# Optimization experiments

Hardware: AMD Instinct MI355X
Metric: run time of the kernel (lower is better)

Reference implementation:

```python
import jax, jax.numpy as jnp
import numpy as np

B, N, F, D, C = 4096, 8, 64, 64, 10  # batch, carriages, phys dim, bond dim, output classes


def setup_inputs() -> dict:
    key = jax.random.key(0)
    k1, k2, k3, k4 = jax.random.split(key, 4)
    scale = 1.0 / np.sqrt(F * D)
    x = jax.random.normal(k1, (B, N, F), dtype=jnp.float32)
    core_first = jax.random.normal(k2, (C, F, D), dtype=jnp.float32) * scale  # A1: (left=1 squeezed, up=C, p=F, right=D)
    cores_mid = jax.random.normal(k3, (N - 2, D, F, D), dtype=jnp.float32) * scale  # A2..A7: (D, up=1 squeezed, F, D)
    core_last = jax.random.normal(k4, (D, F), dtype=jnp.float32) * scale  # A8: (D, up=1, F, right=1 squeezed)
    return {"x": x, "core_first": core_first, "cores_mid": cores_mid, "core_last": core_last}


def reference(x, core_first, cores_mid, core_last):
    # Tensor-train forward: out[s, c] = sum over bond chain of
    #   A1[c, p1, r1] x[s,0,p1] * prod_i A_i[l, p_i, r] x[s,i,p_i] * A_N[l, p_N] x[s,N-1,p_N]
    # First carriage: contract physical leg -> (B, C, D)
    T0 = jnp.einsum('sp,cpr->scr', x[:, 0], core_first)
    # Middle carriages: sequential chain of small bond-dim GEMMs via scan
    xs_mid = jnp.moveaxis(x[:, 1:-1], 1, 0)  # (N-2, B, F)

    def step(T, inp):
        xi, core = inp  # xi: (B, F), core: (D, F, D)
        M = jnp.einsum('sp,lpr->slr', xi, core)  # (B, D, D)
        return jnp.einsum('scl,slr->scr', T, M), None

    T, _ = jax.lax.scan(step, T0, (xs_mid, cores_mid))
    # Last carriage: contract physical and close the chain -> (B, C)
    m_last = jnp.einsum('sp,lp->sl', x[:, -1], core_last)  # (B, D)
    out = jnp.einsum('scl,sl->sc', T, m_last)
    return out
```

## Files before the change

### kernel.cpp

```cpp
#include <hip/hip_runtime.h>


typedef _Float16 half8 __attribute__((ext_vector_type(8)));
typedef _Float16 half4 __attribute__((ext_vector_type(4)));
typedef _Float16 half2v __attribute__((ext_vector_type(2)));
typedef float f32x4 __attribute__((ext_vector_type(4)));

#define LAST_OFF   0
#define MID_OFF    4096
#define MID_SZ     262144
#define FIRST_OFF  1576960
#define N_FRAGS    3208

__global__ __launch_bounds__(256) void tt_swz(
    const float* __restrict__ cf,
    const float* __restrict__ cm,
    const float* __restrict__ cl,
    _Float16* __restrict__ ws)
{
  int gid = blockIdx.x * 256 + threadIdx.x;
  if (gid >= N_FRAGS * 64) return;
  int lane = gid & 63, frag = gid >> 6;
  int quad = lane >> 4, m16 = lane & 15;
  half8 hv;
  _Float16* dst;
  if (frag < 8) {
    int t = frag >> 1, kt = frag & 1;
    int l = t * 16 + m16;
    const float* s = cl + l * 64 + kt * 32 + quad * 8;
#pragma unroll
    for (int j = 0; j < 8; ++j) hv[j] = (_Float16)s[j];
    dst = ws + LAST_OFF + (size_t)((t * 2 + kt) * 64 + lane) * 8;
  } else if (frag < 8 + 3072) {
    int f2 = frag - 8;
    int ci = f2 >> 9, rem = f2 & 511;
    int t = rem >> 1, kt = rem & 1;
    int l = (t & 3) * 16 + m16, p = t >> 2;
    const float* s = cm + (((size_t)ci * 64 + l) * 64 + p) * 64 + kt * 32 + quad * 8;
#pragma unroll
    for (int j = 0; j < 8; ++j) hv[j] = (_Float16)s[j];
    dst = ws + MID_OFF + (size_t)ci * MID_SZ + (size_t)(rem * 64 + lane) * 8;
  } else {
    int f2 = frag - 3080;
    int t = f2 >> 1, kt = f2 & 1;
    int c = m16, p = t;
    if (c < 10) {
      const float* s = cf + ((size_t)(c * 64 + p)) * 64 + kt * 32 + quad * 8;
#pragma unroll
      for (int j = 0; j < 8; ++j) hv[j] = (_Float16)s[j];
    } else {
#pragma unroll
      for (int j = 0; j < 8; ++j) hv[j] = (_Float16)0.f;
    }
    dst = ws + FIRST_OFF + (size_t)((t * 2 + kt) * 64 + lane) * 8;
  }
  *(half8*)dst = hv;
}

__global__ __launch_bounds__(1024) void tt_main(
    const float* __restrict__ x,
    const _Float16* __restrict__ ws,
    float* __restrict__ out)
{
  __shared__ __align__(16) _Float16 Xs[512][33];
  __shared__ __align__(16) _Float16 Vt[4][32][72];
  __shared__ __align__(16) _Float16 Vc[32][72];
  const int tid = threadIdx.x;
  const int w = tid >> 6, lane = tid & 63;
  const int quad = lane >> 4, sl = lane & 15;
  const int blk = blockIdx.x;

  {
    const float* xb = x + (size_t)blk * 32 * 512;
    int s = tid >> 5, q = tid & 31;
#pragma unroll
    for (int k = 0; k < 4; ++k) {
      int f4 = q + 32 * k;
      float4 v = *(const float4*)(xb + (size_t)s * 512 + (size_t)f4 * 4);
      int row = f4 * 4;
      Xs[row + 0][s] = (_Float16)v.x;
      Xs[row + 1][s] = (_Float16)v.y;
      Xs[row + 2][s] = (_Float16)v.z;
      Xs[row + 3][s] = (_Float16)v.w;
    }
    _Float16* vz = &Vt[2][0][0];
    for (int idx = tid; idx < 2 * 32 * 72; idx += 1024) vz[idx] = (_Float16)0.f;
  }
  __syncthreads();

  {
    int st = w >> 3, kt = (w >> 2) & 1, tt = w & 3;
    half8 b;
#pragma unroll
    for (int j = 0; j < 8; ++j)
      b[j] = Xs[448 + kt * 32 + quad * 8 + j][st * 16 + sl];
    half8 a = *(const half8*)(ws + LAST_OFF + (size_t)((tt * 2 + kt) * 64 + lane) * 8);
    f32x4 d = {0.f, 0.f, 0.f, 0.f};
    d = __builtin_amdgcn_mfma_f32_16x16x32_f16(a, b, d, 0, 0, 0);
    half4 hv;
#pragma unroll
    for (int r = 0; r < 4; ++r) hv[r] = (_Float16)d[r];
    *(half4*)&Vt[kt][st * 16 + sl][tt * 16 + quad * 4] = hv;
  }
  __syncthreads();
  {
    int s = tid >> 5, rp = tid & 31;
    float r0 = 0.f, r1 = 0.f;
#pragma unroll
    for (int p = 0; p < 4; ++p) {
      half2v h = *(const half2v*)&Vt[p][s][rp * 2];
      r0 += (float)h[0]; r1 += (float)h[1];
    }
    half2v o; o[0] = (_Float16)r0; o[1] = (_Float16)r1;
    *(half2v*)&Vc[s][rp * 2] = o;
  }
  __syncthreads();

  const int g = w & 3, part = w >> 2;
  for (int step = 0; step < 6; ++step) {
    int ci = 5 - step;
    half8 b00 = *(const half8*)&Vc[sl][quad * 8];
    half8 b01 = *(const half8*)&Vc[sl][32 + quad * 8];
    half8 b10 = *(const half8*)&Vc[16 + sl][quad * 8];
    half8 b11 = *(const half8*)&Vc[16 + sl][32 + quad * 8];
    const _Float16* wl = ws + MID_OFF + (size_t)ci * MID_SZ
                       + (size_t)w * 1024 + (size_t)lane * 8;
    float c00 = 0.f, c01 = 0.f, c02 = 0.f, c03 = 0.f;
    float c10 = 0.f, c11 = 0.f, c12 = 0.f, c13 = 0.f;
    const int xrow = (ci + 1) * 64;
#pragma unroll 4
    for (int j = 0; j < 16; ++j) {
      int t = j * 16 + w;
      int p = t >> 2;
      const _Float16* fp = wl + (size_t)j * 16384;
      half8 A0 = *(const half8*)fp;
      half8 A1 = *(const half8*)(fp + 512);
      f32x4 d0 = {0.f, 0.f, 0.f, 0.f}, d1 = {0.f, 0.f, 0.f, 0.f};
      d0 = __builtin_amdgcn_mfma_f32_16x16x32_f16(A0, b00, d0, 0, 0, 0);
      d0 = __builtin_amdgcn_mfma_f32_16x16x32_f16(A1, b01, d0, 0, 0, 0);
      d1 = __builtin_amdgcn_mfma_f32_16x16x32_f16(A0, b10, d1, 0, 0, 0);
      d1 = __builtin_amdgcn_mfma_f32_16x16x32_f16(A1, b11, d1, 0, 0, 0);
      float xv0 = (float)Xs[xrow + p][sl];
      float xv1 = (float)Xs[xrow + p][16 + sl];
      c00 += xv0 * d0[0]; c01 += xv0 * d0[1]; c02 += xv0 * d0[2]; c03 += xv0 * d0[3];
      c10 += xv1 * d1[0]; c11 += xv1 * d1[1]; c12 += xv1 * d1[2]; c13 += xv1 * d1[3];
    }
    half4 h0, h1;
    h0[0] = (_Float16)c00; h0[1] = (_Float16)c01; h0[2] = (_Float16)c02; h0[3] = (_Float16)c03;
    h1[0] = (_Float16)c10; h1[1] = (_Float16)c11; h1[2] = (_Float16)c12; h1[3] = (_Float16)c13;
    *(half4*)&Vt[part][sl][g * 16 + quad * 4] = h0;
    *(half4*)&Vt[part][16 + sl][g * 16 + quad * 4] = h1;
    __syncthreads();
    {
      int s = tid >> 5, rp = tid & 31;
      float r0 = 0.f, r1 = 0.f;
#pragma unroll
      for (int p = 0; p < 4; ++p) {
        half2v h = *(const half2v*)&Vt[p][s][rp * 2];
        r0 += (float)h[0]; r1 += (float)h[1];
      }
      half2v o; o[0] = (_Float16)r0; o[1] = (_Float16)r1;
      *(half2v*)&Vc[s][rp * 2] = o;
    }
    __syncthreads();
  }

  float* Red = (float*)&Vt[0][0][0];
  if (w < 8) {
    half8 b00 = *(const half8*)&Vc[sl][quad * 8];
    half8 b01 = *(const half8*)&Vc[sl][32 + quad * 8];
    half8 b10 = *(const half8*)&Vc[16 + sl][quad * 8];
    half8 b11 = *(const half8*)&Vc[16 + sl][32 + quad * 8];
    float f00 = 0.f, f01 = 0.f, f02 = 0.f, f03 = 0.f;
    float f10 = 0.f, f11 = 0.f, f12 = 0.f, f13 = 0.f;
#pragma unroll
    for (int j = 0; j < 8; ++j) {
      int t = j * 8 + w;
      const _Float16* fp = ws + FIRST_OFF + (size_t)t * 1024 + (size_t)lane * 8;
      half8 A0 = *(const half8*)fp;
      half8 A1 = *(const half8*)(fp + 512);
      f32x4 d0 = {0.f, 0.f, 0.f, 0.f}, d1 = {0.f, 0.f, 0.f, 0.f};
      d0 = __builtin_amdgcn_mfma_f32_16x16x32_f16(A0, b00, d0, 0, 0, 0);
      d0 = __builtin_amdgcn_mfma_f32_16x16x32_f16(A1, b01, d0, 0, 0, 0);
      d1 = __builtin_amdgcn_mfma_f32_16x16x32_f16(A0, b10, d1, 0, 0, 0);
      d1 = __builtin_amdgcn_mfma_f32_16x16x32_f16(A1, b11, d1, 0, 0, 0);
      float xv0 = (float)Xs[t][sl];
      float xv1 = (float)Xs[t][16 + sl];
      f00 += xv0 * d0[0]; f01 += xv0 * d0[1]; f02 += xv0 * d0[2]; f03 += xv0 * d0[3];
      f10 += xv1 * d1[0]; f11 += xv1 * d1[1]; f12 += xv1 * d1[2]; f13 += xv1 * d1[3];
    }
    float a0[4] = {f00, f01, f02, f03};
    float a1[4] = {f10, f11, f12, f13};
#pragma unroll
    for (int r = 0; r < 4; ++r) {
      int c = quad * 4 + r;
      if (c < 10) {
        Red[(w * 10 + c) * 32 + sl] = a0[r];
        Red[(w * 10 + c) * 32 + 16 + sl] = a1[r];
      }
    }
  }
  __syncthreads();
  if (tid < 320) {
    int c = tid >> 5, s = tid & 31;
    float sum = 0.f;
#pragma unroll
    for (int ww = 0; ww < 8; ++ww) sum += Red[(ww * 10 + c) * 32 + s];
    out[((size_t)blk * 32 + s) * 10 + c] = sum;
  }
}

extern "C" void kernel_launch(void* const* d_in, const int* in_sizes, int n_in,
                              void* d_out, int out_size, void* d_ws, size_t ws_size,
                              hipStream_t stream) {
  const float* x  = (const float*)d_in[0];
  const float* cf = (const float*)d_in[1];
  const float* cm = (const float*)d_in[2];
  const float* cl = (const float*)d_in[3];
  _Float16* ws = (_Float16*)d_ws;
  float* out = (float*)d_out;
  tt_swz<<<dim3((N_FRAGS * 64 + 255) / 256), dim3(256), 0, stream>>>(cf, cm, cl, ws);
  tt_main<<<dim3(128), dim3(1024), 0, stream>>>(x, ws, out);
}
```

Before: 101.5 us.

## Split each batch tile's bond contraction across four cooperating blocks with flag sync

Each group of 64 samples is now handled by four blocks, and each block computes one quarter of the physical-index reduction at every chain step. Partial results go to global workspace and are combined after polling per-step flags, with a fallback that recomputes any quarter that does not arrive in time. The final stage uses atomic adds into an output that the prep kernel zeroes. This spreads the work over 256 blocks instead of 128 to raise parallelism, at the cost of inter-block spin synchronization, extra global traffic and the risk that co-resident scheduling is not guaranteed.

```diff
diff --git a/kernel.cpp b/kernel.cpp
--- a/kernel.cpp
+++ b/kernel.cpp
@@ -3,210 +3,322 @@
 
 typedef _Float16 half8 __attribute__((ext_vector_type(8)));
 typedef _Float16 half4 __attribute__((ext_vector_type(4)));
-typedef _Float16 half2v __attribute__((ext_vector_type(2)));
 typedef float f32x4 __attribute__((ext_vector_type(4)));
+typedef unsigned long long u64;
 
 #define LAST_OFF   0
 #define MID_OFF    4096
 #define MID_SZ     262144
 #define FIRST_OFF  1576960
 #define N_FRAGS    3208
+#define PART_BYTE_OFF (16u << 20)
+#define FLAG_BYTE_OFF (48u << 20)
+#define POLL_MAX   20000
+#define SWZ_TOTAL  (N_FRAGS * 64 + 40960 + 1536)
 
 __global__ __launch_bounds__(256) void tt_swz(
     const float* __restrict__ cf,
     const float* __restrict__ cm,
     const float* __restrict__ cl,
-    _Float16* __restrict__ ws)
+    _Float16* __restrict__ ws,
+    float* __restrict__ out)
 {
   int gid = blockIdx.x * 256 + threadIdx.x;
-  if (gid >= N_FRAGS * 64) return;
-  int lane = gid & 63, frag = gid >> 6;
-  int quad = lane >> 4, m16 = lane & 15;
-  half8 hv;
-  _Float16* dst;
-  if (frag < 8) {
-    int t = frag >> 1, kt = frag & 1;
-    int l = t * 16 + m16;
-    const float* s = cl + l * 64 + kt * 32 + quad * 8;
-#pragma unroll
-    for (int j = 0; j < 8; ++j) hv[j] = (_Float16)s[j];
-    dst = ws + LAST_OFF + (size_t)((t * 2 + kt) * 64 + lane) * 8;
-  } else if (frag < 8 + 3072) {
-    int f2 = frag - 8;
-    int ci = f2 >> 9, rem = f2 & 511;
-    int t = rem >> 1, kt = rem & 1;
-    int l = (t & 3) * 16 + m16, p = t >> 2;
-    const float* s = cm + (((size_t)ci * 64 + l) * 64 + p) * 64 + kt * 32 + quad * 8;
-#pragma unroll
-    for (int j = 0; j < 8; ++j) hv[j] = (_Float16)s[j];
-    dst = ws + MID_OFF + (size_t)ci * MID_SZ + (size_t)(rem * 64 + lane) * 8;
-  } else {
-    int f2 = frag - 3080;
-    int t = f2 >> 1, kt = f2 & 1;
-    int c = m16, p = t;
-    if (c < 10) {
-      const float* s = cf + ((size_t)(c * 64 + p)) * 64 + kt * 32 + quad * 8;
+  if (gid < N_FRAGS * 64) {
+    int lane = gid & 63, frag = gid >> 6;
+    int quad = lane >> 4, m16 = lane & 15;
+    half8 hv;
+    _Float16* dst;
+    if (frag < 8) {
+      int t = frag >> 1, kt = frag & 1;
+      int l = t * 16 + m16;
+      const float* s = cl + l * 64 + kt * 32 + quad * 8;
 #pragma unroll
       for (int j = 0; j < 8; ++j) hv[j] = (_Float16)s[j];
+      dst = ws + LAST_OFF + (size_t)((t * 2 + kt) * 64 + lane) * 8;
+    } else if (frag < 8 + 3072) {
+      int f2 = frag - 8;
+      int ci = f2 >> 9, rem = f2 & 511;
+      int t = rem >> 1, kt = rem & 1;
+      int l = (t & 3) * 16 + m16, p = t >> 2;
+      const float* s = cm + (((size_t)ci * 64 + l) * 64 + p) * 64 + kt * 32 + quad * 8;
+#pragma unroll
+      for (int j = 0; j < 8; ++j) hv[j] = (_Float16)s[j];
+      dst = ws + MID_OFF + (size_t)ci * MID_SZ + (size_t)(rem * 64 + lane) * 8;
     } else {
-#pragma unroll
-      for (int j = 0; j < 8; ++j) hv[j] = (_Float16)0.f;
-    }
-    dst = ws + FIRST_OFF + (size_t)((t * 2 + kt) * 64 + lane) * 8;
-  }
-  *(half8*)dst = hv;
+      int f2 = frag - 3080;
+      int t = f2 >> 1, kt = f2 & 1;
+      int c = m16, p = t;
+      if (c < 10) {
+        const float* s = cf + ((size_t)(c * 64 + p)) * 64 + kt * 32 + quad * 8;
+#pragma unroll
+        for (int j = 0; j < 8; ++j) hv[j] = (_Float16)s[j];
+      } else {
+#pragma unroll
+        for (int j = 0; j < 8; ++j) hv[j] = (_Float16)0.f;
+      }
+      dst = ws + FIRST_OFF + (size_t)((t * 2 + kt) * 64 + lane) * 8;
+    }
+    *(half8*)dst = hv;
+    return;
+  }
+  int e = gid - N_FRAGS * 64;
+  if (e < 40960) { out[e] = 0.f; return; }
+  e -= 40960;
+  if (e < 1536) {
+    unsigned* flags = (unsigned*)((char*)ws + FLAG_BYTE_OFF);
+    __hip_atomic_store(&flags[e], 0u, __ATOMIC_RELAXED, __HIP_MEMORY_SCOPE_AGENT);
+  }
 }
 
-__global__ __launch_bounds__(1024) void tt_main(
+__global__ __launch_bounds__(512) void tt_main(
     const float* __restrict__ x,
-    const _Float16* __restrict__ ws,
+    _Float16* __restrict__ ws,
     float* __restrict__ out)
 {
-  __shared__ __align__(16) _Float16 Xs[512][33];
-  __shared__ __align__(16) _Float16 Vt[4][32][72];
-  __shared__ __align__(16) _Float16 Vc[32][72];
+  __shared__ __align__(16) _Float16 Xs[64][72];
+  __shared__ __align__(16) _Float16 Vc[64][72];
+  __shared__ __align__(16) _Float16 Vt[2][64][72];
+  __shared__ float RedL[10][68];
+  __shared__ int status[4];
+
   const int tid = threadIdx.x;
   const int w = tid >> 6, lane = tid & 63;
   const int quad = lane >> 4, sl = lane & 15;
-  const int blk = blockIdx.x;
-
-  {
-    const float* xb = x + (size_t)blk * 32 * 512;
-    int s = tid >> 5, q = tid & 31;
-#pragma unroll
-    for (int k = 0; k < 4; ++k) {
-      int f4 = q + 32 * k;
-      float4 v = *(const float4*)(xb + (size_t)s * 512 + (size_t)f4 * 4);
-      int row = f4 * 4;
-      Xs[row + 0][s] = (_Float16)v.x;
-      Xs[row + 1][s] = (_Float16)v.y;
-      Xs[row + 2][s] = (_Float16)v.z;
-      Xs[row + 3][s] = (_Float16)v.w;
-    }
-    _Float16* vz = &Vt[2][0][0];
-    for (int idx = tid; idx < 2 * 32 * 72; idx += 1024) vz[idx] = (_Float16)0.f;
-  }
-  __syncthreads();
-
-  {
-    int st = w >> 3, kt = (w >> 2) & 1, tt = w & 3;
-    half8 b;
-#pragma unroll
-    for (int j = 0; j < 8; ++j)
-      b[j] = Xs[448 + kt * 32 + quad * 8 + j][st * 16 + sl];
-    half8 a = *(const half8*)(ws + LAST_OFF + (size_t)((tt * 2 + kt) * 64 + lane) * 8);
-    f32x4 d = {0.f, 0.f, 0.f, 0.f};
-    d = __builtin_amdgcn_mfma_f32_16x16x32_f16(a, b, d, 0, 0, 0);
-    half4 hv;
-#pragma unroll
-    for (int r = 0; r < 4; ++r) hv[r] = (_Float16)d[r];
-    *(half4*)&Vt[kt][st * 16 + sl][tt * 16 + quad * 4] = hv;
-  }
+  const int b = blockIdx.x;
+  const int q = (b >> 3) & 3;
+  const int g = (b & 7) | ((b >> 5) << 3);
+  const int s0 = g * 64;
+  const int pg = w >> 2, lt = w & 3;
+  const int cs = tid >> 3, l8 = (tid & 7) * 8;
+
+  unsigned* flags = (unsigned*)((char*)ws + FLAG_BYTE_OFF);
+
+  auto stageX = [&](int n) {
+    int s = tid >> 3, p8 = (tid & 7) * 8;
+    const float* src = x + ((size_t)(s0 + s) * 8 + n) * 64 + p8;
+    float4 a = *(const float4*)src;
+    float4 b4 = *(const float4*)(src + 4);
+    half8 h;
+    h[0] = (_Float16)a.x;  h[1] = (_Float16)a.y;
+    h[2] = (_Float16)a.z;  h[3] = (_Float16)a.w;
+    h[4] = (_Float16)b4.x; h[5] = (_Float16)b4.y;
+    h[6] = (_Float16)b4.z; h[7] = (_Float16)b4.w;
+    *(half8*)&Xs[s][p8] = h;
+  };
+
+  auto accum_quarter = [&](int qq, int ci, half8 (&B)[4][2], float (&c)[4][4]) {
+    const _Float16* wl = ws + MID_OFF + (size_t)ci * MID_SZ
+                       + (size_t)((qq * 64 + w) * 1024) + (size_t)lane * 8;
+#pragma unroll 4
+    for (int j = 0; j < 8; ++j) {
+      const _Float16* fp = wl + (size_t)j * 8192;
+      half8 A0 = *(const half8*)fp;
+      half8 A1 = *(const half8*)(fp + 512);
+      f32x4 d0 = {0.f, 0.f, 0.f, 0.f}, d1 = d0, d2 = d0, d3 = d0;
+      d0 = __builtin_amdgcn_mfma_f32_16x16x32_f16(A0, B[0][0], d0, 0, 0, 0);
+      d0 = __builtin_amdgcn_mfma_f32_16x16x32_f16(A1, B[0][1], d0, 0, 0, 0);
+      d1 = __builtin_amdgcn_mfma_f32_16x16x32_f16(A0, B[1][0], d1, 0, 0, 0);
+      d1 = __builtin_amdgcn_mfma_f32_16x16x32_f16(A1, B[1][1], d1, 0, 0, 0);
+      d2 = __builtin_amdgcn_mfma_f32_16x16x32_f16(A0, B[2][0], d2, 0, 0, 0);
+      d2 = __builtin_amdgcn_mfma_f32_16x16x32_f16(A1, B[2][1], d2, 0, 0, 0);
+      d3 = __builtin_amdgcn_mfma_f32_16x16x32_f16(A0, B[3][0], d3, 0, 0, 0);
+      d3 = __builtin_amdgcn_mfma_f32_16x16x32_f16(A1, B[3][1], d3, 0, 0, 0);
+      int p = qq * 16 + 2 * j + pg;
+      float xv0 = (float)Xs[sl][p];
+      float xv1 = (float)Xs[16 + sl][p];
+      float xv2 = (float)Xs[32 + sl][p];
+      float xv3 = (float)Xs[48 + sl][p];
+#pragma unroll
+      for (int r2 = 0; r2 < 4; ++r2) {
+        c[0][r2] += xv0 * d0[r2];
+        c[1][r2] += xv1 * d1[r2];
+        c[2][r2] += xv2 * d2[r2];
+        c[3][r2] += xv3 * d3[r2];
+      }
+    }
+  };
+
+  stageX(7);
   __syncthreads();
   {
-    int s = tid >> 5, rp = tid & 31;
-    float r0 = 0.f, r1 = 0.f;
-#pragma unroll
-    for (int p = 0; p < 4; ++p) {
-      half2v h = *(const half2v*)&Vt[p][s][rp * 2];
-      r0 += (float)h[0]; r1 += (float)h[1];
-    }
-    half2v o; o[0] = (_Float16)r0; o[1] = (_Float16)r1;
-    *(half2v*)&Vc[s][rp * 2] = o;
+    int sh = w >> 2, vlt = w & 3;
+    half8 A0 = *(const half8*)(ws + LAST_OFF + (size_t)((vlt * 2 + 0) * 64 + lane) * 8);
+    half8 A1 = *(const half8*)(ws + LAST_OFF + (size_t)((vlt * 2 + 1) * 64 + lane) * 8);
+#pragma unroll
+    for (int st2 = 0; st2 < 2; ++st2) {
+      int st = sh * 2 + st2;
+      half8 b0 = *(const half8*)&Xs[st * 16 + sl][quad * 8];
+      half8 b1 = *(const half8*)&Xs[st * 16 + sl][32 + quad * 8];
+      f32x4 d = {0.f, 0.f, 0.f, 0.f};
+      d = __builtin_amdgcn_mfma_f32_16x16x32_f16(A0, b0, d, 0, 0, 0);
+      d = __builtin_amdgcn_mfma_f32_16x16x32_f16(A1, b1, d, 0, 0, 0);
+      half4 hv;
+#pragma unroll
+      for (int r2 = 0; r2 < 4; ++r2) hv[r2] = (_Float16)d[r2];
+      *(half4*)&Vc[st * 16 + sl][vlt * 16 + quad * 4] = hv;
+    }
   }
   __syncthreads();
 
-  const int g = w & 3, part = w >> 2;
   for (int step = 0; step < 6; ++step) {
-    int ci = 5 - step;
-    half8 b00 = *(const half8*)&Vc[sl][quad * 8];
-    half8 b01 = *(const half8*)&Vc[sl][32 + quad * 8];
-    half8 b10 = *(const half8*)&Vc[16 + sl][quad * 8];
-    half8 b11 = *(const half8*)&Vc[16 + sl][32 + quad * 8];
-    const _Float16* wl = ws + MID_OFF + (size_t)ci * MID_SZ
-                       + (size_t)w * 1024 + (size_t)lane * 8;
-    float c00 = 0.f, c01 = 0.f, c02 = 0.f, c03 = 0.f;
-    float c10 = 0.f, c11 = 0.f, c12 = 0.f, c13 = 0.f;
-    const int xrow = (ci + 1) * 64;
-#pragma unroll 4
-    for (int j = 0; j < 16; ++j) {
-      int t = j * 16 + w;
-      int p = t >> 2;
-      const _Float16* fp = wl + (size_t)j * 16384;
+    const int ci = 5 - step;
+    stageX(ci + 1);
+    __syncthreads();
+
+    half8 B[4][2];
+#pragma unroll
+    for (int st = 0; st < 4; ++st) {
+      B[st][0] = *(const half8*)&Vc[st * 16 + sl][quad * 8];
+      B[st][1] = *(const half8*)&Vc[st * 16 + sl][32 + quad * 8];
+    }
+    float c[4][4] = {};
+    accum_quarter(q, ci, B, c);
+
+#pragma unroll
+    for (int st = 0; st < 4; ++st) {
+      half4 hv;
+#pragma unroll
+      for (int r2 = 0; r2 < 4; ++r2) hv[r2] = (_Float16)c[st][r2];
+      *(half4*)&Vt[pg][st * 16 + sl][lt * 16 + quad * 4] = hv;
+    }
+    __syncthreads();
+
+    half8 t0 = *(const half8*)&Vt[0][cs][l8];
+    half8 t1 = *(const half8*)&Vt[1][cs][l8];
+    float own[8];
+#pragma unroll
+    for (int k2 = 0; k2 < 8; ++k2) own[k2] = (float)t0[k2] + (float)t1[k2];
+    {
+      union { u64 u[2]; half8 h; } pu;
+#pragma unroll
+      for (int k2 = 0; k2 < 8; ++k2) pu.h[k2] = (_Float16)own[k2];
+      u64* dst = (u64*)((char*)ws + PART_BYTE_OFF
+                 + ((size_t)((step * 64 + g) * 4 + q) * 8192)
+                 + (size_t)(cs * 64 + l8) * 2);
+      __hip_atomic_store(dst + 0, pu.u[0], __ATOMIC_RELAXED, __HIP_MEMORY_SCOPE_AGENT);
+      __hip_atomic_store(dst + 1, pu.u[1], __ATOMIC_RELAXED, __HIP_MEMORY_SCOPE_AGENT);
+    }
+    __threadfence();
+    __syncthreads();
+
+    if (tid == 0) {
+      unsigned base = (unsigned)(step * 64 + g) * 4;
+      __hip_atomic_store(&flags[base + q], 1u, __ATOMIC_RELEASE, __HIP_MEMORY_SCOPE_AGENT);
+      int got[4] = {0, 0, 0, 0};
+      got[q] = 2;
+      for (int it = 0;; ++it) {
+        int done = 1;
+#pragma unroll
+        for (int qq = 0; qq < 4; ++qq) {
+          if (!got[qq]) {
+            got[qq] = (int)__hip_atomic_load(&flags[base + qq], __ATOMIC_ACQUIRE,
+                                             __HIP_MEMORY_SCOPE_AGENT);
+            if (!got[qq]) done = 0;
+          }
+        }
+        if (done || it >= POLL_MAX) break;
+        __builtin_amdgcn_s_sleep(2);
+      }
+      status[0] = got[0]; status[1] = got[1];
+      status[2] = got[2]; status[3] = got[3];
+    }
+    __syncthreads();
+
+    int nmiss = (status[0] == 0) + (status[1] == 0) + (status[2] == 0) + (status[3] == 0);
+    if (__builtin_expect(nmiss > 0, 0)) {
+      for (int qq = 0; qq < 4; ++qq)
+        if (status[qq] == 0) accum_quarter(qq, ci, B, c);
+#pragma unroll
+      for (int st = 0; st < 4; ++st) {
+        half4 hv;
+#pragma unroll
+        for (int r2 = 0; r2 < 4; ++r2) hv[r2] = (_Float16)c[st][r2];
+        *(half4*)&Vt[pg][st * 16 + sl][lt * 16 + quad * 4] = hv;
+      }
+      __syncthreads();
+      half8 u0 = *(const half8*)&Vt[0][cs][l8];
+      half8 u1 = *(const half8*)&Vt[1][cs][l8];
+#pragma unroll
+      for (int k2 = 0; k2 < 8; ++k2) own[k2] = (float)u0[k2] + (float)u1[k2];
+    }
+
+    float acc[8];
+#pragma unroll
+    for (int k2 = 0; k2 < 8; ++k2) acc[k2] = own[k2];
+#pragma unroll
+    for (int qq = 0; qq < 4; ++qq) {
+      if (qq != q && status[qq] != 0) {
+        const u64* srcp = (const u64*)((const char*)ws + PART_BYTE_OFF
+                     + ((size_t)((step * 64 + g) * 4 + qq) * 8192)
+                     + (size_t)(cs * 64 + l8) * 2);
+        union { u64 u[2]; half8 h; } pu;
+        pu.u[0] = __hip_atomic_load(srcp + 0, __ATOMIC_RELAXED, __HIP_MEMORY_SCOPE_AGENT);
+        pu.u[1] = __hip_atomic_load(srcp + 1, __ATOMIC_RELAXED, __HIP_MEMORY_SCOPE_AGENT);
+#pragma unroll
+        for (int k2 = 0; k2 < 8; ++k2) acc[k2] += (float)pu.h[k2];
+      }
+    }
+    half8 nh;
+#pragma unroll
+    for (int k2 = 0; k2 < 8; ++k2) nh[k2] = (_Float16)acc[k2];
+    *(half8*)&Vc[cs][l8] = nh;
+    __syncthreads();
+  }
+
+  stageX(0);
+  {
+    float* rl = &RedL[0][0];
+    for (int i = tid; i < 10 * 68; i += 512) rl[i] = 0.f;
+  }
+  __syncthreads();
+  {
+    half8 B[4][2];
+#pragma unroll
+    for (int st = 0; st < 4; ++st) {
+      B[st][0] = *(const half8*)&Vc[st * 16 + sl][quad * 8];
+      B[st][1] = *(const half8*)&Vc[st * 16 + sl][32 + quad * 8];
+    }
+    float c[4][4] = {};
+#pragma unroll
+    for (int j = 0; j < 2; ++j) {
+      int t = q * 16 + j * 8 + w;
+      const _Float16* fp = ws + FIRST_OFF + (size_t)(t * 2) * 512 + (size_t)lane * 8;
       half8 A0 = *(const half8*)fp;
       half8 A1 = *(const half8*)(fp + 512);
-      f32x4 d0 = {0.f, 0.f, 0.f, 0.f}, d1 = {0.f, 0.f, 0.f, 0.f};
-      d0 = __builtin_amdgcn_mfma_f32_16x16x32_f16(A0, b00, d0, 0, 0, 0);
-      d0 = __builtin_amdgcn_mfma_f32_16x16x32_f16(A1, b01, d0, 0, 0, 0);
-      d1 = __builtin_amdgcn_mfma_f32_16x16x32_f16(A0, b10, d1, 0, 0, 0);
-      d1 = __builtin_amdgcn_mfma_f32_16x16x32_f16(A1, b11, d1, 0, 0, 0);
-      float xv0 = (float)Xs[xrow + p][sl];
-      float xv1 = (float)Xs[xrow + p][16 + sl];
-      c00 += xv0 * d0[0]; c01 += xv0 * d0[1]; c02 += xv0 * d0[2]; c03 += xv0 * d0[3];
-      c10 += xv1 * d1[0]; c11 += xv1 * d1[1]; c12 += xv1 * d1[2]; c13 += xv1 * d1[3];
-    }
-    half4 h0, h1;
-    h0[0] = (_Float16)c00; h0[1] = (_Float16)c01; h0[2] = (_Float16)c02; h0[3] = (_Float16)c03;
-    h1[0] = (_Float16)c10; h1[1] = (_Float16)c11; h1[2] = (_Float16)c12; h1[3] = (_Float16)c13;
-    *(half4*)&Vt[part][sl][g * 16 + quad * 4] = h0;
-    *(half4*)&Vt[part][16 + sl][g * 16 + quad * 4] = h1;
-    __syncthreads();
-    {
-      int s = tid >> 5, rp = tid & 31;
-      float r0 = 0.f, r1 = 0.f;
-#pragma unroll
-      for (int p = 0; p < 4; ++p) {
-        half2v h = *(const half2v*)&Vt[p][s][rp * 2];
-        r0 += (float)h[0]; r1 += (float)h[1];
-      }
-      half2v o; o[0] = (_Float16)r0; o[1] = (_Float16)r1;
-      *(half2v*)&Vc[s][rp * 2] = o;
-    }
-    __syncthreads();
-  }
-
-  float* Red = (float*)&Vt[0][0][0];
-  if (w < 8) {
-    half8 b00 = *(const half8*)&Vc[sl][quad * 8];
-    half8 b01 = *(const half8*)&Vc[sl][32 + quad * 8];
-    half8 b10 = *(const half8*)&Vc[16 + sl][quad * 8];
-    half8 b11 = *(const half8*)&Vc[16 + sl][32 + quad * 8];
-    float f00 = 0.f, f01 = 0.f, f02 = 0.f, f03 = 0.f;
-    float f10 = 0.f, f11 = 0.f, f12 = 0.f, f13 = 0.f;
-#pragma unroll
-    for (int j = 0; j < 8; ++j) {
-      int t = j * 8 + w;
-      const _Float16* fp = ws + FIRST_OFF + (size_t)t * 1024 + (size_t)lane * 8;
-      half8 A0 = *(const half8*)fp;
-      half8 A1 = *(const half8*)(fp + 512);
-      f32x4 d0 = {0.f, 0.f, 0.f, 0.f}, d1 = {0.f, 0.f, 0.f, 0.f};
-      d0 = __builtin_amdgcn_mfma_f32_16x16x32_f16(A0, b00, d0, 0, 0, 0);
-      d0 = __builtin_amdgcn_mfma_f32_16x16x32_f16(A1, b01, d0, 0, 0, 0);
-      d1 = __builtin_amdgcn_mfma_f32_16x16x32_f16(A0, b10, d1, 0, 0, 0);
-      d1 = __builtin_amdgcn_mfma_f32_16x16x32_f16(A1, b11, d1, 0, 0, 0);
-      float xv0 = (float)Xs[t][sl];
-      float xv1 = (float)Xs[t][16 + sl];
-      f00 += xv0 * d0[0]; f01 += xv0 * d0[1]; f02 += xv0 * d0[2]; f03 += xv0 * d0[3];
-      f10 += xv1 * d1[0]; f11 += xv1 * d1[1]; f12 += xv1 * d1[2]; f13 += xv1 * d1[3];
-    }
-    float a0[4] = {f00, f01, f02, f03};
-    float a1[4] = {f10, f11, f12, f13};
-#pragma unroll
-    for (int r = 0; r < 4; ++r) {
-      int c = quad * 4 + r;
-      if (c < 10) {
-        Red[(w * 10 + c) * 32 + sl] = a0[r];
-        Red[(w * 10 + c) * 32 + 16 + sl] = a1[r];
-      }
-    }
+      f32x4 d0 = {0.f, 0.f, 0.f, 0.f}, d1 = d0, d2 = d0, d3 = d0;
+      d0 = __builtin_amdgcn_mfma_f32_16x16x32_f16(A0, B[0][0], d0, 0, 0, 0);
+      d0 = __builtin_amdgcn_mfma_f32_16x16x32_f16(A1, B[0][1], d0, 0, 0, 0);
+      d1 = __builtin_amdgcn_mfma_f32_16x16x32_f16(A0, B[1][0], d1, 0, 0, 0);
+      d1 = __builtin_amdgcn_mfma_f32_16x16x32_f16(A1, B[1][1], d1, 0, 0, 0);
+      d2 = __builtin_amdgcn_mfma_f32_16x16x32_f16(A0, B[2][0], d2, 0, 0, 0);
+      d2 = __builtin_amdgcn_mfma_f32_16x16x32_f16(A1, B[2][1], d2, 0, 0, 0);
+      d3 = __builtin_amdgcn_mfma_f32_16x16x32_f16(A0, B[3][0], d3, 0, 0, 0);
+      d3 = __builtin_amdgcn_mfma_f32_16x16x32_f16(A1, B[3][1], d3, 0, 0, 0);
+      float xv0 = (float)Xs[sl][t];
+      float xv1 = (float)Xs[16 + sl][t];
+      float xv2 = (float)Xs[32 + sl][t];
+      float xv3 = (float)Xs[48 + sl][t];
+#pragma unroll
+      for (int r2 = 0; r2 < 4; ++r2) {
+        c[0][r2] += xv0 * d0[r2];
+        c[1][r2] += xv1 * d1[r2];
+        c[2][r2] += xv2 * d2[r2];
+        c[3][r2] += xv3 * d3[r2];
+      }
+    }
+#pragma unroll
+    for (int st = 0; st < 4; ++st)
+#pragma unroll
+      for (int r2 = 0; r2 < 4; ++r2) {
+        int cc = quad * 4 + r2;
+        if (cc < 10) atomicAdd(&RedL[cc][st * 16 + sl], c[st][r2]);
+      }
   }
   __syncthreads();
-  if (tid < 320) {
-    int c = tid >> 5, s = tid & 31;
-    float sum = 0.f;
-#pragma unroll
-    for (int ww = 0; ww < 8; ++ww) sum += Red[(ww * 10 + c) * 32 + s];
-    out[((size_t)blk * 32 + s) * 10 + c] = sum;
+  for (int i = tid; i < 640; i += 512) {
+    int cc = i >> 6, s = i & 63;
+    atomicAdd(&out[(size_t)(s0 + s) * 10 + cc], RedL[cc][s]);
   }
 }
 
@@ -219,6 +331,6 @@
   const float* cl = (const float*)d_in[3];
   _Float16* ws = (_Float16*)d_ws;
   float* out = (float*)d_out;
-  tt_swz<<<dim3((N_FRAGS * 64 + 255) / 256), dim3(256), 0, stream>>>(cf, cm, cl, ws);
-  tt_main<<<dim3(128), dim3(1024), 0, stream>>>(x, ws, out);
+  tt_swz<<<dim3((SWZ_TOTAL + 255) / 256), dim3(256), 0, stream>>>(cf, cm, cl, ws, out);
+  tt_main<<<dim3(256), dim3(512), 0, stream>>>(x, ws, out);
 }
```

New measurement: 339.1 us. +234.0%, slower.

## Process 64 samples per block to reuse core fragments, software-pipeline loads

Applied to the files above, without the earlier changes.

Each block now handles 64 samples instead of 32, so every fp16 core fragment loaded from global memory feeds four MFMA column tiles instead of two, halving weight traffic per sample. The grid shrinks from 128 to 64 blocks. The mid-carriage loop is double-buffered with explicit prefetch of the next fragment pair, and the partial-sum reductions use wider half4 accesses. The trade-off is fewer blocks (only 64 of the GPU's CUs busy), more registers per thread, and larger LDS use.

```diff
diff --git a/kernel.cpp b/kernel.cpp
--- a/kernel.cpp
+++ b/kernel.cpp
@@ -3,7 +3,6 @@
 
 typedef _Float16 half8 __attribute__((ext_vector_type(8)));
 typedef _Float16 half4 __attribute__((ext_vector_type(4)));
-typedef _Float16 half2v __attribute__((ext_vector_type(2)));
 typedef float f32x4 __attribute__((ext_vector_type(4)));
 
 #define LAST_OFF   0
@@ -62,20 +61,22 @@
     const _Float16* __restrict__ ws,
     float* __restrict__ out)
 {
-  __shared__ __align__(16) _Float16 Xs[512][33];
-  __shared__ __align__(16) _Float16 Vt[4][32][72];
-  __shared__ __align__(16) _Float16 Vc[32][72];
+  __shared__ __align__(16) _Float16 Xs[512][66];
+  __shared__ __align__(16) _Float16 Vt[4][64][72];
+  __shared__ __align__(16) _Float16 Vc[64][72];
   const int tid = threadIdx.x;
   const int w = tid >> 6, lane = tid & 63;
   const int quad = lane >> 4, sl = lane & 15;
   const int blk = blockIdx.x;
+  const int g = w & 3, part = w >> 2;
+  const int cs2 = tid >> 4, rp4 = (tid & 15) * 4;
 
   {
-    const float* xb = x + (size_t)blk * 32 * 512;
-    int s = tid >> 5, q = tid & 31;
-#pragma unroll
-    for (int k = 0; k < 4; ++k) {
-      int f4 = q + 32 * k;
+    const float* xb = x + (size_t)blk * 64 * 512;
+    int s = tid >> 4, q = tid & 15;
+#pragma unroll
+    for (int k = 0; k < 8; ++k) {
+      int f4 = q + 16 * k;
       float4 v = *(const float4*)(xb + (size_t)s * 512 + (size_t)f4 * 4);
       int row = f4 * 4;
       Xs[row + 0][s] = (_Float16)v.x;
@@ -83,130 +84,164 @@
       Xs[row + 2][s] = (_Float16)v.z;
       Xs[row + 3][s] = (_Float16)v.w;
     }
-    _Float16* vz = &Vt[2][0][0];
-    for (int idx = tid; idx < 2 * 32 * 72; idx += 1024) vz[idx] = (_Float16)0.f;
   }
   __syncthreads();
 
   {
-    int st = w >> 3, kt = (w >> 2) & 1, tt = w & 3;
-    half8 b;
-#pragma unroll
-    for (int j = 0; j < 8; ++j)
-      b[j] = Xs[448 + kt * 32 + quad * 8 + j][st * 16 + sl];
+    int sh = w >> 3, kt = (w >> 2) & 1, tt = w & 3;
     half8 a = *(const half8*)(ws + LAST_OFF + (size_t)((tt * 2 + kt) * 64 + lane) * 8);
-    f32x4 d = {0.f, 0.f, 0.f, 0.f};
-    d = __builtin_amdgcn_mfma_f32_16x16x32_f16(a, b, d, 0, 0, 0);
-    half4 hv;
-#pragma unroll
-    for (int r = 0; r < 4; ++r) hv[r] = (_Float16)d[r];
-    *(half4*)&Vt[kt][st * 16 + sl][tt * 16 + quad * 4] = hv;
+#pragma unroll
+    for (int st2 = 0; st2 < 2; ++st2) {
+      int st = sh * 2 + st2;
+      half8 b;
+#pragma unroll
+      for (int j = 0; j < 8; ++j)
+        b[j] = Xs[448 + kt * 32 + quad * 8 + j][st * 16 + sl];
+      f32x4 d = {0.f, 0.f, 0.f, 0.f};
+      d = __builtin_amdgcn_mfma_f32_16x16x32_f16(a, b, d, 0, 0, 0);
+      half4 hv;
+#pragma unroll
+      for (int r = 0; r < 4; ++r) hv[r] = (_Float16)d[r];
+      *(half4*)&Vt[kt][st * 16 + sl][tt * 16 + quad * 4] = hv;
+    }
   }
   __syncthreads();
   {
-    int s = tid >> 5, rp = tid & 31;
-    float r0 = 0.f, r1 = 0.f;
-#pragma unroll
-    for (int p = 0; p < 4; ++p) {
-      half2v h = *(const half2v*)&Vt[p][s][rp * 2];
-      r0 += (float)h[0]; r1 += (float)h[1];
-    }
-    half2v o; o[0] = (_Float16)r0; o[1] = (_Float16)r1;
-    *(half2v*)&Vc[s][rp * 2] = o;
-  }
-  __syncthreads();
-
-  const int g = w & 3, part = w >> 2;
+    half4 t0 = *(const half4*)&Vt[0][cs2][rp4];
+    half4 t1 = *(const half4*)&Vt[1][cs2][rp4];
+    half4 o;
+#pragma unroll
+    for (int r = 0; r < 4; ++r) o[r] = (_Float16)((float)t0[r] + (float)t1[r]);
+    *(half4*)&Vc[cs2][rp4] = o;
+  }
+  __syncthreads();
+
+#define MID_LOAD(Xa, Xb, J) { \
+    const _Float16* fp_ = wl + (size_t)(J) * 16384; \
+    Xa = *(const half8*)fp_; \
+    Xb = *(const half8*)(fp_ + 512); }
+
+#define MID_MFMA(Xa, Xb, J) { \
+    int p_ = (J) * 4 + part; \
+    f32x4 d0 = {0.f,0.f,0.f,0.f}, d1 = d0, d2 = d0, d3 = d0; \
+    d0 = __builtin_amdgcn_mfma_f32_16x16x32_f16(Xa, B00, d0, 0, 0, 0); \
+    d0 = __builtin_amdgcn_mfma_f32_16x16x32_f16(Xb, B01, d0, 0, 0, 0); \
+    d1 = __builtin_amdgcn_mfma_f32_16x16x32_f16(Xa, B10, d1, 0, 0, 0); \
+    d1 = __builtin_amdgcn_mfma_f32_16x16x32_f16(Xb, B11, d1, 0, 0, 0); \
+    d2 = __builtin_amdgcn_mfma_f32_16x16x32_f16(Xa, B20, d2, 0, 0, 0); \
+    d2 = __builtin_amdgcn_mfma_f32_16x16x32_f16(Xb, B21, d2, 0, 0, 0); \
+    d3 = __builtin_amdgcn_mfma_f32_16x16x32_f16(Xa, B30, d3, 0, 0, 0); \
+    d3 = __builtin_amdgcn_mfma_f32_16x16x32_f16(Xb, B31, d3, 0, 0, 0); \
+    float xv0 = (float)Xs[xrow + p_][sl]; \
+    float xv1 = (float)Xs[xrow + p_][16 + sl]; \
+    float xv2 = (float)Xs[xrow + p_][32 + sl]; \
+    float xv3 = (float)Xs[xrow + p_][48 + sl]; \
+    c0 += d0 * xv0; c1 += d1 * xv1; c2 += d2 * xv2; c3 += d3 * xv3; }
+
   for (int step = 0; step < 6; ++step) {
     int ci = 5 - step;
-    half8 b00 = *(const half8*)&Vc[sl][quad * 8];
-    half8 b01 = *(const half8*)&Vc[sl][32 + quad * 8];
-    half8 b10 = *(const half8*)&Vc[16 + sl][quad * 8];
-    half8 b11 = *(const half8*)&Vc[16 + sl][32 + quad * 8];
+    half8 B00 = *(const half8*)&Vc[sl][quad * 8];
+    half8 B01 = *(const half8*)&Vc[sl][32 + quad * 8];
+    half8 B10 = *(const half8*)&Vc[16 + sl][quad * 8];
+    half8 B11 = *(const half8*)&Vc[16 + sl][32 + quad * 8];
+    half8 B20 = *(const half8*)&Vc[32 + sl][quad * 8];
+    half8 B21 = *(const half8*)&Vc[32 + sl][32 + quad * 8];
+    half8 B30 = *(const half8*)&Vc[48 + sl][quad * 8];
+    half8 B31 = *(const half8*)&Vc[48 + sl][32 + quad * 8];
     const _Float16* wl = ws + MID_OFF + (size_t)ci * MID_SZ
                        + (size_t)w * 1024 + (size_t)lane * 8;
-    float c00 = 0.f, c01 = 0.f, c02 = 0.f, c03 = 0.f;
-    float c10 = 0.f, c11 = 0.f, c12 = 0.f, c13 = 0.f;
     const int xrow = (ci + 1) * 64;
-#pragma unroll 4
-    for (int j = 0; j < 16; ++j) {
-      int t = j * 16 + w;
-      int p = t >> 2;
-      const _Float16* fp = wl + (size_t)j * 16384;
-      half8 A0 = *(const half8*)fp;
-      half8 A1 = *(const half8*)(fp + 512);
-      f32x4 d0 = {0.f, 0.f, 0.f, 0.f}, d1 = {0.f, 0.f, 0.f, 0.f};
-      d0 = __builtin_amdgcn_mfma_f32_16x16x32_f16(A0, b00, d0, 0, 0, 0);
-      d0 = __builtin_amdgcn_mfma_f32_16x16x32_f16(A1, b01, d0, 0, 0, 0);
-      d1 = __builtin_amdgcn_mfma_f32_16x16x32_f16(A0, b10, d1, 0, 0, 0);
-      d1 = __builtin_amdgcn_mfma_f32_16x16x32_f16(A1, b11, d1, 0, 0, 0);
-      float xv0 = (float)Xs[xrow + p][sl];
-      float xv1 = (float)Xs[xrow + p][16 + sl];
-      c00 += xv0 * d0[0]; c01 += xv0 * d0[1]; c02 += xv0 * d0[2]; c03 += xv0 * d0[3];
-      c10 += xv1 * d1[0]; c11 += xv1 * d1[1]; c12 += xv1 * d1[2]; c13 += xv1 * d1[3];
-    }
-    half4 h0, h1;
-    h0[0] = (_Float16)c00; h0[1] = (_Float16)c01; h0[2] = (_Float16)c02; h0[3] = (_Float16)c03;
-    h1[0] = (_Float16)c10; h1[1] = (_Float16)c11; h1[2] = (_Float16)c12; h1[3] = (_Float16)c13;
-    *(half4*)&Vt[part][sl][g * 16 + quad * 4] = h0;
-    *(half4*)&Vt[part][16 + sl][g * 16 + quad * 4] = h1;
+    f32x4 c0 = {0.f,0.f,0.f,0.f}, c1 = c0, c2 = c0, c3 = c0;
+    half8 PA0, PA1, QA0, QA1;
+    MID_LOAD(PA0, PA1, 0)
+#pragma unroll
+    for (int jj = 0; jj < 8; ++jj) {
+      const int j0 = jj * 2, j1 = jj * 2 + 1;
+      MID_LOAD(QA0, QA1, j1)
+      MID_MFMA(PA0, PA1, j0)
+      if (j1 + 1 < 16) MID_LOAD(PA0, PA1, j1 + 1)
+      MID_MFMA(QA0, QA1, j1)
+    }
+    {
+      half4 h;
+#pragma unroll
+      for (int r = 0; r < 4; ++r) h[r] = (_Float16)c0[r];
+      *(half4*)&Vt[part][sl][g * 16 + quad * 4] = h;
+#pragma unroll
+      for (int r = 0; r < 4; ++r) h[r] = (_Float16)c1[r];
+      *(half4*)&Vt[part][16 + sl][g * 16 + quad * 4] = h;
+#pragma unroll
+      for (int r = 0; r < 4; ++r) h[r] = (_Float16)c2[r];
+      *(half4*)&Vt[part][32 + sl][g * 16 + quad * 4] = h;
+#pragma unroll
+      for (int r = 0; r < 4; ++r) h[r] = (_Float16)c3[r];
+      *(half4*)&Vt[part][48 + sl][g * 16 + quad * 4] = h;
+    }
     __syncthreads();
     {
-      int s = tid >> 5, rp = tid & 31;
-      float r0 = 0.f, r1 = 0.f;
-#pragma unroll
-      for (int p = 0; p < 4; ++p) {
-        half2v h = *(const half2v*)&Vt[p][s][rp * 2];
-        r0 += (float)h[0]; r1 += (float)h[1];
-      }
-      half2v o; o[0] = (_Float16)r0; o[1] = (_Float16)r1;
-      *(half2v*)&Vc[s][rp * 2] = o;
+      half4 t0 = *(const half4*)&Vt[0][cs2][rp4];
+      half4 t1 = *(const half4*)&Vt[1][cs2][rp4];
+      half4 t2 = *(const half4*)&Vt[2][cs2][rp4];
+      half4 t3 = *(const half4*)&Vt[3][cs2][rp4];
+      half4 o;
+#pragma unroll
+      for (int r = 0; r < 4; ++r)
+        o[r] = (_Float16)(((float)t0[r] + (float)t1[r]) + ((float)t2[r] + (float)t3[r]));
+      *(half4*)&Vc[cs2][rp4] = o;
     }
     __syncthreads();
   }
 
   float* Red = (float*)&Vt[0][0][0];
   if (w < 8) {
-    half8 b00 = *(const half8*)&Vc[sl][quad * 8];
-    half8 b01 = *(const half8*)&Vc[sl][32 + quad * 8];
-    half8 b10 = *(const half8*)&Vc[16 + sl][quad * 8];
-    half8 b11 = *(const half8*)&Vc[16 + sl][32 + quad * 8];
-    float f00 = 0.f, f01 = 0.f, f02 = 0.f, f03 = 0.f;
-    float f10 = 0.f, f11 = 0.f, f12 = 0.f, f13 = 0.f;
+    half8 B00 = *(const half8*)&Vc[sl][quad * 8];
+    half8 B01 = *(const half8*)&Vc[sl][32 + quad * 8];
+    half8 B10 = *(const half8*)&Vc[16 + sl][quad * 8];
+    half8 B11 = *(const half8*)&Vc[16 + sl][32 + quad * 8];
+    half8 B20 = *(const half8*)&Vc[32 + sl][quad * 8];
+    half8 B21 = *(const half8*)&Vc[32 + sl][32 + quad * 8];
+    half8 B30 = *(const half8*)&Vc[48 + sl][quad * 8];
+    half8 B31 = *(const half8*)&Vc[48 + sl][32 + quad * 8];
+    f32x4 c0 = {0.f,0.f,0.f,0.f}, c1 = c0, c2 = c0, c3 = c0;
 #pragma unroll
     for (int j = 0; j < 8; ++j) {
       int t = j * 8 + w;
       const _Float16* fp = ws + FIRST_OFF + (size_t)t * 1024 + (size_t)lane * 8;
       half8 A0 = *(const half8*)fp;
       half8 A1 = *(const half8*)(fp + 512);
-      f32x4 d0 = {0.f, 0.f, 0.f, 0.f}, d1 = {0.f, 0.f, 0.f, 0.f};
-      d0 = __builtin_amdgcn_mfma_f32_16x16x32_f16(A0, b00, d0, 0, 0, 0);
-      d0 = __builtin_amdgcn_mfma_f32_16x16x32_f16(A1, b01, d0, 0, 0, 0);
-      d1 = __builtin_amdgcn_mfma_f32_16x16x32_f16(A0, b10, d1, 0, 0, 0);
-      d1 = __builtin_amdgcn_mfma_f32_16x16x32_f16(A1, b11, d1, 0, 0, 0);
+      f32x4 d0 = {0.f,0.f,0.f,0.f}, d1 = d0, d2 = d0, d3 = d0;
+      d0 = __builtin_amdgcn_mfma_f32_16x16x32_f16(A0, B00, d0, 0, 0, 0);
+      d0 = __builtin_amdgcn_mfma_f32_16x16x32_f16(A1, B01, d0, 0, 0, 0);
+      d1 = __builtin_amdgcn_mfma_f32_16x16x32_f16(A0, B10, d1, 0, 0, 0);
+      d1 = __builtin_amdgcn_mfma_f32_16x16x32_f16(A1, B11, d1, 0, 0, 0);
+      d2 = __builtin_amdgcn_mfma_f32_16x16x32_f16(A0, B20, d2, 0, 0, 0);
+      d2 = __builtin_amdgcn_mfma_f32_16x16x32_f16(A1, B21, d2, 0, 0, 0);
+      d3 = __builtin_amdgcn_mfma_f32_16x16x32_f16(A0, B30, d3, 0, 0, 0);
+      d3 = __builtin_amdgcn_mfma_f32_16x16x32_f16(A1, B31, d3, 0, 0, 0);
       float xv0 = (float)Xs[t][sl];
       float xv1 = (float)Xs[t][16 + sl];
-      f00 += xv0 * d0[0]; f01 += xv0 * d0[1]; f02 += xv0 * d0[2]; f03 += xv0 * d0[3];
-      f10 += xv1 * d1[0]; f11 += xv1 * d1[1]; f12 += xv1 * d1[2]; f13 += xv1 * d1[3];
-    }
-    float a0[4] = {f00, f01, f02, f03};
-    float a1[4] = {f10, f11, f12, f13};
+      float xv2 = (float)Xs[t][32 + sl];
+      float xv3 = (float)Xs[t][48 + sl];
+      c0 += d0 * xv0; c1 += d1 * xv1; c2 += d2 * xv2; c3 += d3 * xv3;
+    }
 #pragma unroll
     for (int r = 0; r < 4; ++r) {
       int c = quad * 4 + r;
       if (c < 10) {
-        Red[(w * 10 + c) * 32 + sl] = a0[r];
-        Red[(w * 10 + c) * 32 + 16 + sl] = a1[r];
+        Red[(w * 10 + c) * 64 + sl]      = c0[r];
+        Red[(w * 10 + c) * 64 + 16 + sl] = c1[r];
+        Red[(w * 10 + c) * 64 + 32 + sl] = c2[r];
+        Red[(w * 10 + c) * 64 + 48 + sl] = c3[r];
       }
     }
   }
   __syncthreads();
-  if (tid < 320) {
-    int c = tid >> 5, s = tid & 31;
+  if (tid < 640) {
+    int c = tid >> 6, s = tid & 63;
     float sum = 0.f;
 #pragma unroll
-    for (int ww = 0; ww < 8; ++ww) sum += Red[(ww * 10 + c) * 32 + s];
-    out[((size_t)blk * 32 + s) * 10 + c] = sum;
+    for (int ww = 0; ww < 8; ++ww) sum += Red[(ww * 10 + c) * 64 + s];
+    out[((size_t)blk * 64 + s) * 10 + c] = sum;
   }
 }
 
@@ -220,5 +255,5 @@
   _Float16* ws = (_Float16*)d_ws;
   float* out = (float*)d_out;
   tt_swz<<<dim3((N_FRAGS * 64 + 255) / 256), dim3(256), 0, stream>>>(cf, cm, cl, ws);
-  tt_main<<<dim3(128), dim3(1024), 0, stream>>>(x, ws, out);
+  tt_main<<<dim3(64), dim3(1024), 0, stream>>>(x, ws, out);
 }
```

Measured after the change: 117.9 us. 1.16x slower.

## Stream middle-core fragments through a triple-buffered LDS ring with async global-to-LDS loads

Applied to the files above, without the earlier changes.

The middle-carriage loop now reads its fp16 core fragments from a three-slot LDS ring instead of straight from global memory. Loads are issued two chunks ahead with global_load_lds and guarded by explicit vmcnt waits and raw barriers. Plain __syncthreads are replaced with an lgkmcnt wait plus s_barrier, and the loop is fully unrolled. The aim is to hide global latency behind the MFMA work. In exchange it adds a block-wide barrier on every inner iteration and about 96KB of extra shared memory per block, and correctness depends on the hand-written wait counts.

```diff
diff --git a/kernel.cpp b/kernel.cpp
--- a/kernel.cpp
+++ b/kernel.cpp
@@ -11,6 +11,15 @@
 #define MID_SZ     262144
 #define FIRST_OFF  1576960
 #define N_FRAGS    3208
+#define CH         16384
+
+typedef __attribute__((address_space(3))) void lvoid_t;
+typedef const __attribute__((address_space(1))) void gvoid_t;
+
+#define LBAR() do { \
+    asm volatile("s_waitcnt lgkmcnt(0)" ::: "memory"); \
+    __builtin_amdgcn_s_barrier(); \
+    __builtin_amdgcn_sched_barrier(0); } while (0)
 
 __global__ __launch_bounds__(256) void tt_swz(
     const float* __restrict__ cf,
@@ -62,6 +71,7 @@
     const _Float16* __restrict__ ws,
     float* __restrict__ out)
 {
+  __shared__ __align__(16) _Float16 Aring[3 * CH];
   __shared__ __align__(16) _Float16 Xs[512][33];
   __shared__ __align__(16) _Float16 Vt[4][32][72];
   __shared__ __align__(16) _Float16 Vc[32][72];
@@ -69,6 +79,17 @@
   const int w = tid >> 6, lane = tid & 63;
   const int quad = lane >> 4, sl = lane & 15;
   const int blk = blockIdx.x;
+
+  auto stage = [&](int J, _Float16* dstbase) {
+    int stp = J >> 4, jj = J & 15;
+    const _Float16* gb = ws + MID_OFF + (size_t)(5 - stp) * MID_SZ + (size_t)jj * CH;
+    const _Float16* g0 = gb + (size_t)tid * 8;
+    const _Float16* g1 = gb + (size_t)(tid + 1024) * 8;
+    _Float16* l0 = dstbase + w * 512;
+    _Float16* l1 = dstbase + 8192 + w * 512;
+    __builtin_amdgcn_global_load_lds((gvoid_t*)g0, (lvoid_t*)l0, 16, 0, 0);
+    __builtin_amdgcn_global_load_lds((gvoid_t*)g1, (lvoid_t*)l1, 16, 0, 0);
+  };
 
   {
     const float* xb = x + (size_t)blk * 32 * 512;
@@ -86,7 +107,7 @@
     _Float16* vz = &Vt[2][0][0];
     for (int idx = tid; idx < 2 * 32 * 72; idx += 1024) vz[idx] = (_Float16)0.f;
   }
-  __syncthreads();
+  LBAR();
 
   {
     int st = w >> 3, kt = (w >> 2) & 1, tt = w & 3;
@@ -102,7 +123,9 @@
     for (int r = 0; r < 4; ++r) hv[r] = (_Float16)d[r];
     *(half4*)&Vt[kt][st * 16 + sl][tt * 16 + quad * 4] = hv;
   }
-  __syncthreads();
+  stage(0, Aring);
+  stage(1, Aring + CH);
+  LBAR();
   {
     int s = tid >> 5, rp = tid & 31;
     float r0 = 0.f, r1 = 0.f;
@@ -114,43 +137,51 @@
     half2v o; o[0] = (_Float16)r0; o[1] = (_Float16)r1;
     *(half2v*)&Vc[s][rp * 2] = o;
   }
-  __syncthreads();
+  LBAR();
 
   const int g = w & 3, part = w >> 2;
+  _Float16* pc = Aring;
+  _Float16* pn = Aring + CH;
+  _Float16* ps = Aring + 2 * CH;
+
   for (int step = 0; step < 6; ++step) {
     int ci = 5 - step;
     half8 b00 = *(const half8*)&Vc[sl][quad * 8];
     half8 b01 = *(const half8*)&Vc[sl][32 + quad * 8];
     half8 b10 = *(const half8*)&Vc[16 + sl][quad * 8];
     half8 b11 = *(const half8*)&Vc[16 + sl][32 + quad * 8];
-    const _Float16* wl = ws + MID_OFF + (size_t)ci * MID_SZ
-                       + (size_t)w * 1024 + (size_t)lane * 8;
     float c00 = 0.f, c01 = 0.f, c02 = 0.f, c03 = 0.f;
     float c10 = 0.f, c11 = 0.f, c12 = 0.f, c13 = 0.f;
     const int xrow = (ci + 1) * 64;
-#pragma unroll 4
+#pragma unroll
     for (int j = 0; j < 16; ++j) {
-      int t = j * 16 + w;
-      int p = t >> 2;
-      const _Float16* fp = wl + (size_t)j * 16384;
-      half8 A0 = *(const half8*)fp;
-      half8 A1 = *(const half8*)(fp + 512);
+      const int J = step * 16 + j;
+      if (J <= 94) asm volatile("s_waitcnt vmcnt(2)" ::: "memory");
+      else         asm volatile("s_waitcnt vmcnt(0)" ::: "memory");
+      __builtin_amdgcn_s_barrier();
+      __builtin_amdgcn_sched_barrier(0);
+      const _Float16* ap = pc + w * 1024 + lane * 8;
+      half8 A0 = *(const half8*)ap;
+      half8 A1 = *(const half8*)(ap + 512);
+      if (J + 2 < 96) stage(J + 2, ps);
+      int p = (j * 16 + w) >> 2;
+      float xv0 = (float)Xs[xrow + p][sl];
+      float xv1 = (float)Xs[xrow + p][16 + sl];
       f32x4 d0 = {0.f, 0.f, 0.f, 0.f}, d1 = {0.f, 0.f, 0.f, 0.f};
       d0 = __builtin_amdgcn_mfma_f32_16x16x32_f16(A0, b00, d0, 0, 0, 0);
       d0 = __builtin_amdgcn_mfma_f32_16x16x32_f16(A1, b01, d0, 0, 0, 0);
       d1 = __builtin_amdgcn_mfma_f32_16x16x32_f16(A0, b10, d1, 0, 0, 0);
       d1 = __builtin_amdgcn_mfma_f32_16x16x32_f16(A1, b11, d1, 0, 0, 0);
-      float xv0 = (float)Xs[xrow + p][sl];
-      float xv1 = (float)Xs[xrow + p][16 + sl];
       c00 += xv0 * d0[0]; c01 += xv0 * d0[1]; c02 += xv0 * d0[2]; c03 += xv0 * d0[3];
       c10 += xv1 * d1[0]; c11 += xv1 * d1[1]; c12 += xv1 * d1[2]; c13 += xv1 * d1[3];
+      _Float16* t = pc; pc = pn; pn = ps; ps = t;
     }
     half4 h0, h1;
     h0[0] = (_Float16)c00; h0[1] = (_Float16)c01; h0[2] = (_Float16)c02; h0[3] = (_Float16)c03;
     h1[0] = (_Float16)c10; h1[1] = (_Float16)c11; h1[2] = (_Float16)c12; h1[3] = (_Float16)c13;
     *(half4*)&Vt[part][sl][g * 16 + quad * 4] = h0;
     *(half4*)&Vt[part][16 + sl][g * 16 + quad * 4] = h1;
-    __syncthreads();
+    LBAR();
     {
       int s = tid >> 5, rp = tid & 31;
       float r0 = 0.f, r1 = 0.f;
@@ -162,7 +193,7 @@
       half2v o; o[0] = (_Float16)r0; o[1] = (_Float16)r1;
       *(half2v*)&Vc[s][rp * 2] = o;
     }
-    __syncthreads();
+    LBAR();
   }
 
   float* Red = (float*)&Vt[0][0][0];
@@ -179,13 +210,13 @@
       const _Float16* fp = ws + FIRST_OFF + (size_t)t * 1024 + (size_t)lane * 8;
       half8 A0 = *(const half8*)fp;
       half8 A1 = *(const half8*)(fp + 512);
+      float xv0 = (float)Xs[t][sl];
+      float xv1 = (float)Xs[t][16 + sl];
       f32x4 d0 = {0.f, 0.f, 0.f, 0.f}, d1 = {0.f, 0.f, 0.f, 0.f};
       d0 = __builtin_amdgcn_mfma_f32_16x16x32_f16(A0, b00, d0, 0, 0, 0);
       d0 = __builtin_amdgcn_mfma_f32_16x16x32_f16(A1, b01, d0, 0, 0, 0);
       d1 = __builtin_amdgcn_mfma_f32_16x16x32_f16(A0, b10, d1, 0, 0, 0);
       d1 = __builtin_amdgcn_mfma_f32_16x16x32_f16(A1, b11, d1, 0, 0, 0);
-      float xv0 = (float)Xs[t][sl];
-      float xv1 = (float)Xs[t][16 + sl];
       f00 += xv0 * d0[0]; f01 += xv0 * d0[1]; f02 += xv0 * d0[2]; f03 += xv0 * d0[3];
       f10 += xv1 * d1[0]; f11 += xv1 * d1[1]; f12 += xv1 * d1[2]; f13 += xv1 * d1[3];
     }
@@ -200,7 +231,7 @@
       }
     }
   }
-  __syncthreads();
+  LBAR();
   if (tid < 320) {
     int c = tid >> 5, s = tid & 31;
     float sum = 0.f;
```

After: 110.3 us. 1.09x slower.
